# Performance work log

Measured on AMD Instinct MI355X. Metric: run time of the kernel, lower is better.

Reference implementation:

```python
import jax, jax.numpy as jnp
import numpy as np

N = 100000
E = 800000
D_IN = 128
D_H = 128
D_OUT = 40
L = 16
ALPHA = 0.1
THETA = 0.5
BN_EPS = 1e-5


def setup_inputs() -> dict:
    key = jax.random.key(0)
    ks = jax.random.split(key, 8)
    x = jax.random.normal(ks[0], (N, D_IN), dtype=jnp.float32)
    edge_row = jax.random.randint(ks[1], (E,), 0, N, dtype=jnp.int32)
    edge_col = jax.random.randint(ks[2], (E,), 0, N, dtype=jnp.int32)
    edge_weight = jax.random.uniform(ks[3], (E,), dtype=jnp.float32) / 8.0  # ~normalized adj values
    W_in = jax.random.normal(ks[4], (D_IN, D_H), dtype=jnp.float32) / np.sqrt(D_IN)
    b_in = jnp.zeros((D_H,), jnp.float32)
    conv_W = jax.random.normal(ks[5], (L, D_H, D_H), dtype=jnp.float32) / np.sqrt(D_H)
    bn_gamma = jnp.ones((L, D_H), jnp.float32)
    bn_beta = jnp.zeros((L, D_H), jnp.float32)
    W_out = jax.random.normal(ks[6], (D_H, D_OUT), dtype=jnp.float32) / np.sqrt(D_H)
    b_out = jnp.zeros((D_OUT,), jnp.float32)
    return {"x": x, "edge_weight": edge_weight, "W_in": W_in, "b_in": b_in,
            "conv_W": conv_W, "bn_gamma": bn_gamma, "bn_beta": bn_beta,
            "W_out": W_out, "b_out": b_out,
            "edge_row": edge_row, "edge_col": edge_col}


def reference(x, edge_weight, W_in, b_in, conv_W, bn_gamma, bn_beta, W_out, b_out, edge_row, edge_col):
    # input linear + relu (dropout p=0 -> identity)
    x0 = jax.nn.relu(x @ W_in + b_in)            # [N, D_H]
    # GCN2Conv beta coefficients: log(theta/layer + 1), layer = 1..L
    betas = jnp.log(THETA / jnp.arange(1, L + 1, dtype=jnp.float32) + 1.0)

    def spmm(h):
        # out[i] = sum_{e: row[e]=i} w[e] * h[col[e]]
        msgs = edge_weight[:, None] * h[edge_col]     # [E, D_H]
        return jax.ops.segment_sum(msgs, edge_row, num_segments=N)

    def layer(h, params):
        W, g, bb, beta = params
        a = spmm(h)                                   # propagate
        a = (1.0 - ALPHA) * a + ALPHA * x0            # initial-residual mix
        a = (1.0 - beta) * a + beta * (a @ W)         # shared-weights identity mapping
        mu = jnp.mean(a, axis=0)                      # BatchNorm1d (training stats)
        var = jnp.var(a, axis=0)
        a = (a - mu) * jax.lax.rsqrt(var + BN_EPS) * g + bb
        a = a + h                                     # residual
        return jax.nn.relu(a), None

    xL, _ = jax.lax.scan(layer, x0, (conv_W, bn_gamma, bn_beta, betas))
    return xL @ W_out + b_out                         # [N, D_OUT]
```

## Files before the change

kernel.cpp:

```cpp
#include <hip/hip_runtime.h>
#include <math.h>

#define NN 100000
#define EE 800000
#define DH 128
#define NL 16
#define GEMM_GRID 1563
#define SG_GRID 782
#define NSLOT 32

typedef __bf16 bf16x8 __attribute__((ext_vector_type(8)));
typedef float f32x4 __attribute__((ext_vector_type(4)));

__global__ void k_hist(const int* __restrict__ row, int* __restrict__ cnt) {
    int e = blockIdx.x * 256 + threadIdx.x;
    if (e < EE) atomicAdd(&cnt[__builtin_nontemporal_load(&row[e])], 1);
}

__global__ void k_scan1(const int* __restrict__ cnt, int* __restrict__ rp, int* __restrict__ part) {
    __shared__ int buf[512];
    int tid = threadIdx.x;
    int i = blockIdx.x * 512 + tid;
    int v = (i < NN) ? cnt[i] : 0;
    buf[tid] = v;
    __syncthreads();
    for (int off = 1; off < 512; off <<= 1) {
        int x = (tid >= off) ? buf[tid - off] : 0;
        __syncthreads();
        buf[tid] += x;
        __syncthreads();
    }
    if (i < NN) rp[i] = buf[tid] - v;
    if (tid == 511) part[blockIdx.x] = buf[511];
}

__global__ void k_scan2(int* __restrict__ part, int nparts) {
    __shared__ int buf[256];
    int tid = threadIdx.x;
    int v = (tid < nparts) ? part[tid] : 0;
    buf[tid] = v;
    __syncthreads();
    for (int off = 1; off < 256; off <<= 1) {
        int x = (tid >= off) ? buf[tid - off] : 0;
        __syncthreads();
        buf[tid] += x;
        __syncthreads();
    }
    if (tid < nparts) part[tid] = buf[tid] - v;
}

__global__ void k_scan3(int* __restrict__ rp, const int* __restrict__ part) {
    int i = blockIdx.x * 512 + threadIdx.x;
    if (i < NN) rp[i] += part[blockIdx.x];
    if (i == 0) rp[NN] = EE;
}

__global__ void k_dhist(const int* __restrict__ cnt, int* __restrict__ dbin) {
    __shared__ int lb[64];
    int tid = threadIdx.x;
    if (tid < 64) lb[tid] = 0;
    __syncthreads();
    int i = blockIdx.x * 256 + tid;
    if (i < NN) {
        int d = cnt[i];
        if (d > 63) d = 63;
        atomicAdd(&lb[63 - d], 1);
    }
    __syncthreads();
    if (tid < 64 && lb[tid]) atomicAdd(&dbin[tid], lb[tid]);
}

__global__ void k_pscan(const int* __restrict__ dbin, int* __restrict__ dpre) {
    if (threadIdx.x == 0) {
        int s = 0;
        for (int i = 0; i < 64; ++i) { dpre[i] = s; s += dbin[i]; }
    }
}

__global__ void k_pscatter(const int* __restrict__ cnt, const int* __restrict__ dpre,
                           int* __restrict__ dfil, int* __restrict__ perm) {
    __shared__ int lcnt[64], lbase[64];
    int tid = threadIdx.x;
    if (tid < 64) lcnt[tid] = 0;
    __syncthreads();
    int i = blockIdx.x * 256 + tid;
    int b = 0, loc = 0;
    bool ok = (i < NN);
    if (ok) {
        int d = cnt[i];
        if (d > 63) d = 63;
        b = 63 - d;
        loc = atomicAdd(&lcnt[b], 1);
    }
    __syncthreads();
    if (tid < 64 && lcnt[tid]) lbase[tid] = atomicAdd(&dfil[tid], lcnt[tid]);
    __syncthreads();
    if (ok) perm[dpre[b] + lbase[b] + loc] = i;
}

__global__ void k_iperm(const int* __restrict__ perm, const int* __restrict__ cnt,
                        int* __restrict__ iperm, int* __restrict__ cnt2) {
    int i = blockIdx.x * 256 + threadIdx.x;
    if (i < NN) {
        int p = perm[i];
        iperm[p] = i;
        cnt2[i] = cnt[p];
    }
}

__global__ void k_fill(const int* __restrict__ row, const int* __restrict__ col,
                       const float* __restrict__ w, const int* __restrict__ rp,
                       const int* __restrict__ iperm,
                       int* __restrict__ fil, int2* __restrict__ ep) {
    int e = blockIdx.x * 256 + threadIdx.x;
    if (e >= EE) return;
    int r = iperm[__builtin_nontemporal_load(&row[e])];
    int c = iperm[__builtin_nontemporal_load(&col[e])];
    float wv = 0.9f * __builtin_nontemporal_load(&w[e]);
    int pos = rp[r] + atomicAdd(&fil[r], 1);
    unsigned long long v = (unsigned long long)(unsigned)c |
                           ((unsigned long long)(unsigned)__float_as_int(wv) << 32);
    __builtin_nontemporal_store(v, (unsigned long long*)&ep[pos]);
}

__global__ void k_prep_w(const float* __restrict__ convW, const float* __restrict__ Win,
                         __bf16* __restrict__ Bhi, __bf16* __restrict__ Blo) {
    int l = blockIdx.x;
    const float* W;
    float beta, ob;
    if (l < NL) {
        beta = logf(0.5f / (float)(l + 1) + 1.0f);
        ob = 1.0f - beta;
        W = convW + (size_t)l * DH * DH;
    } else {
        beta = 1.0f;
        ob = 0.0f;
        W = Win;
    }
    __bf16* bh = Bhi + (size_t)l * DH * DH;
    __bf16* bl = Blo + (size_t)l * DH * DH;
    for (int i = threadIdx.x; i < DH * DH; i += 256) {
        int k = i >> 7, j = i & 127;
        float v = beta * W[i] + ((k == j) ? ob : 0.f);
        __bf16 hv = (__bf16)v;
        int t = j >> 4, n = j & 15, ks = k >> 5, quad = (k >> 3) & 3, e = k & 7;
        int off = ((t * 4 + ks) * 64 + quad * 16 + n) * 8 + e;
        bh[off] = hv;
        bl[off] = (__bf16)(v - (float)hv);
    }
}

__global__ void k_prep_out(const float* __restrict__ Wout, __bf16* __restrict__ Bhi, __bf16* __restrict__ Blo) {
    for (int i = threadIdx.x; i < DH * 48; i += 256) {
        int k = i / 48, j = i % 48;
        float v = (j < 40) ? Wout[k * 40 + j] : 0.f;
        __bf16 hv = (__bf16)v;
        int t = j >> 4, n = j & 15, ks = k >> 5, quad = (k >> 3) & 3, e = k & 7;
        int off = ((t * 4 + ks) * 64 + quad * 16 + n) * 8 + e;
        Bhi[off] = hv;
        Blo[off] = (__bf16)(v - (float)hv);
    }
}

__device__ inline void split8(const float* p, bf16x8& hi, bf16x8& lo) {
    f32x4 v0 = *(const f32x4*)p;
    f32x4 v1 = *(const f32x4*)(p + 4);
#pragma unroll
    for (int j = 0; j < 4; ++j) {
        __bf16 h0 = (__bf16)v0[j];
        hi[j] = h0;
        lo[j] = (__bf16)(v0[j] - (float)h0);
        __bf16 h1 = (__bf16)v1[j];
        hi[4 + j] = h1;
        lo[4 + j] = (__bf16)(v1[j] - (float)h1);
    }
}

#define MFMA(a, b, c) __builtin_amdgcn_mfma_f32_16x16x32_bf16(a, b, c, 0, 0, 0)

__device__ inline float dec_scale(unsigned int sc4, int ks) {
    return __uint_as_float(((sc4 >> (8 * ks)) & 0xffu) << 23);
}

#define DEC_DW(dw, wsv, a0, a1, a2, a3)                         \
    {                                                           \
        a0 = fmaf(wsv, (float)((dw)&0xffu), a0);                \
        a1 = fmaf(wsv, (float)(((dw) >> 8) & 0xffu), a1);       \
        a2 = fmaf(wsv, (float)(((dw) >> 16) & 0xffu), a2);      \
        a3 = fmaf(wsv, (float)((dw) >> 24), a3);                \
    }

#define EDGE_FMA(S4, W, RA, RB)                                       \
    {                                                                 \
        float _w = (W);                                               \
        float _w0 = _w * dec_scale(S4, 0);                            \
        float _w1 = _w * dec_scale(S4, 1);                            \
        float _w2 = _w * dec_scale(S4, 2);                            \
        float _w3 = _w * dec_scale(S4, 3);                            \
        sw0 += _w0; sw1 += _w1; sw2 += _w2; sw3 += _w3;               \
        DEC_DW((RA).x, _w0, acc[0][0], acc[0][1], acc[0][2], acc[0][3]); \
        DEC_DW((RA).y, _w0, acc[0][4], acc[0][5], acc[0][6], acc[0][7]); \
        DEC_DW((RA).z, _w1, acc[1][0], acc[1][1], acc[1][2], acc[1][3]); \
        DEC_DW((RA).w, _w1, acc[1][4], acc[1][5], acc[1][6], acc[1][7]); \
        DEC_DW((RB).x, _w2, acc[2][0], acc[2][1], acc[2][2], acc[2][3]); \
        DEC_DW((RB).y, _w2, acc[2][4], acc[2][5], acc[2][6], acc[2][7]); \
        DEC_DW((RB).z, _w3, acc[3][0], acc[3][1], acc[3][2], acc[3][3]); \
        DEC_DW((RB).w, _w3, acc[3][4], acc[3][5], acc[3][6], acc[3][7]); \
    }

__global__ __launch_bounds__(512, 4) void k_spmm_gemm(const unsigned char* __restrict__ hin8,
                                                      const unsigned char* __restrict__ hinsc,
                                                      const unsigned char* __restrict__ x08,
                                                      const unsigned char* __restrict__ x0sc,
                                                      const int* __restrict__ rp, const int2* __restrict__ ep,
                                                      unsigned char* __restrict__ a8, unsigned char* __restrict__ asc,
                                                      const __bf16* __restrict__ Bhi, const __bf16* __restrict__ Blo,
                                                      float* __restrict__ stats32) {
    __shared__ __bf16 Bs[2 * DH * DH];
    __shared__ float red[2][8][DH];
    int tid = threadIdx.x;
    {
        const f32x4* sh = (const f32x4*)Bhi;
        const f32x4* sl = (const f32x4*)Blo;
        f32x4* dh = (f32x4*)Bs;
        f32x4* dl = (f32x4*)(Bs + DH * DH);
#pragma unroll
        for (int i = 0; i < 4; ++i) {
            dh[tid + i * 512] = sh[tid + i * 512];
            dl[tid + i * 512] = sl[tid + i * 512];
        }
    }

    int wave = tid >> 6, lane = tid & 63;
    int n = lane & 15, quad = lane >> 4;
    int r0 = blockIdx.x * 128 + wave * 16;
    int node = r0 + n;
    int nc = (node < NN) ? node : (NN - 1);

    float acc[4][8];
#pragma unroll
    for (int ks = 0; ks < 4; ++ks)
#pragma unroll
        for (int c = 0; c < 8; ++c) acc[ks][c] = 0.f;
    float sw0 = 0.f, sw1 = 0.f, sw2 = 0.f, sw3 = 0.f;

    unsigned xs4 = *(const unsigned*)&x0sc[(size_t)nc * 4];
    const unsigned char* xb = x08 + (size_t)nc * 128 + quad * 16;
    uint4 xa = *(const uint4*)xb;
    uint4 xc = *(const uint4*)(xb + 64);

    int s = 0, e = 0;
    if (node < NN) { s = rp[node]; e = rp[node + 1]; }
    int cnt = e - s;
    int npairs = cnt >> 1;

    const unsigned char* hb = hin8 + quad * 16;

    int2 cP0, cP1, fP0, fP1;
    unsigned cS0, cS1;
    uint4 cA0, cB0, cA1, cB1;
    if (npairs > 0) {
        cP0 = ep[s]; cP1 = ep[s + 1];
        cS0 = *(const unsigned*)&hinsc[(size_t)cP0.x * 4];
        cS1 = *(const unsigned*)&hinsc[(size_t)cP1.x * 4];
        const unsigned char* b0 = hb + (size_t)cP0.x * 128;
        const unsigned char* b1 = hb + (size_t)cP1.x * 128;
        cA0 = *(const uint4*)b0; cB0 = *(const uint4*)(b0 + 64);
        cA1 = *(const uint4*)b1; cB1 = *(const uint4*)(b1 + 64);
        int jf = s + 2; if (jf > EE - 2) jf = EE - 2;
        fP0 = ep[jf]; fP1 = ep[jf + 1];
    }

    EDGE_FMA(xs4, 0.1f, xa, xc);

    int j = s;
    for (int it = 0; it < npairs; ++it) {
        int j2 = j + 4; if (j2 > EE - 2) j2 = EE - 2;
        int2 eN0 = ep[j2], eN1 = ep[j2 + 1];
        unsigned tS0 = *(const unsigned*)&hinsc[(size_t)fP0.x * 4];
        unsigned tS1 = *(const unsigned*)&hinsc[(size_t)fP1.x * 4];
        const unsigned char* b0 = hb + (size_t)fP0.x * 128;
        const unsigned char* b1 = hb + (size_t)fP1.x * 128;
        uint4 tA0 = *(const uint4*)b0, tB0 = *(const uint4*)(b0 + 64);
        uint4 tA1 = *(const uint4*)b1, tB1 = *(const uint4*)(b1 + 64);
        EDGE_FMA(cS0, __int_as_float(cP0.y), cA0, cB0);
        EDGE_FMA(cS1, __int_as_float(cP1.y), cA1, cB1);
        cP0 = fP0; cP1 = fP1; fP0 = eN0; fP1 = eN1;
        cS0 = tS0; cS1 = tS1;
        cA0 = tA0; cB0 = tB0; cA1 = tA1; cB1 = tB1;
        j += 2;
    }
    if (cnt & 1) {
        int2 pe = ep[e - 1];
        unsigned s4 = *(const unsigned*)&hinsc[(size_t)pe.x * 4];
        const unsigned char* bp = hb + (size_t)pe.x * 128;
        uint4 ra = *(const uint4*)bp, rb = *(const uint4*)(bp + 64);
        EDGE_FMA(s4, __int_as_float(pe.y), ra, rb);
    }

    bf16x8 av[4];
    {
        float sws[4] = {sw0, sw1, sw2, sw3};
#pragma unroll
        for (int ks = 0; ks < 4; ++ks)
#pragma unroll
            for (int c = 0; c < 8; ++c)
                av[ks][c] = (__bf16)(acc[ks][c] - 128.0f * sws[ks]);
    }

    __syncthreads();

    f32x4 gacc[8];
#pragma unroll
    for (int t = 0; t < 8; ++t) gacc[t] = (f32x4){0.f, 0.f, 0.f, 0.f};

#pragma unroll
    for (int ks = 0; ks < 4; ++ks) {
#pragma unroll
        for (int t = 0; t < 8; ++t) {
            int base = ((t * 4 + ks) * 64 + lane) * 8;
            bf16x8 bh = *(const bf16x8*)&Bs[base];
            bf16x8 bl = *(const bf16x8*)&Bs[DH * DH + base];
            gacc[t] = MFMA(av[ks], bh, gacc[t]);
            gacc[t] = MFMA(av[ks], bl, gacc[t]);
        }
    }

    float m[4][4];
#pragma unroll
    for (int r = 0; r < 4; ++r)
#pragma unroll
        for (int g = 0; g < 4; ++g)
            m[r][g] = fmaxf(fabsf(gacc[2 * g][r]), fabsf(gacc[2 * g + 1][r]));
#pragma unroll
    for (int d = 1; d <= 8; d <<= 1)
#pragma unroll
        for (int r = 0; r < 4; ++r)
#pragma unroll
            for (int g = 0; g < 4; ++g)
                m[r][g] = fmaxf(m[r][g], __shfl_xor(m[r][g], d));
    unsigned ebu[4];
    float sinv[4][4];
#pragma unroll
    for (int r = 0; r < 4; ++r) {
        unsigned u32 = 0;
#pragma unroll
        for (int g = 0; g < 4; ++g) {
            unsigned em = (__float_as_uint(m[r][g]) >> 23) & 0xffu;
            unsigned eb;
            float si;
            if (em < 7) { eb = 0; si = 0.f; }
            else { eb = em - 6; si = __uint_as_float((254 - eb) << 23); }
            u32 |= eb << (8 * g);
            sinv[r][g] = si;
        }
        ebu[r] = u32;
    }

#pragma unroll
    for (int t = 0; t < 8; ++t) {
        float sm = 0.f, qq = 0.f;
        int wb = (t >> 2) * 64 + ((((t & 1) << 1) | (n >> 3))) * 16 + ((t >> 1) & 1) * 8 + (n & 7);
#pragma unroll
        for (int r = 0; r < 4; ++r) {
            int row = r0 + quad * 4 + r;
            float v = gacc[t][r];
            if (row < NN) {
                unsigned qv = (unsigned)rintf(fminf(fmaf(v, sinv[r][t >> 1], 128.f), 255.f));
                a8[(size_t)row * 128 + wb] = (unsigned char)qv;
                sm += v;
                qq += v * v;
            }
        }
        sm += __shfl_xor(sm, 16); sm += __shfl_xor(sm, 32);
        qq += __shfl_xor(qq, 16); qq += __shfl_xor(qq, 32);
        if (quad == 0) {
            red[0][wave][t * 16 + n] = sm;
            red[1][wave][t * 16 + n] = qq;
        }
    }
    if (n == 0) {
#pragma unroll
        for (int r = 0; r < 4; ++r) {
            int row = r0 + quad * 4 + r;
            if (row < NN) *(unsigned*)&asc[(size_t)row * 4] = ebu[r];
        }
    }
    __syncthreads();
    if (tid < 256) {
        int which = tid >> 7, jj = tid & 127;
        float tot = 0.f;
#pragma unroll
        for (int w = 0; w < 8; ++w) tot += red[which][w][jj];
        atomicAdd(&stats32[(size_t)(blockIdx.x & (NSLOT - 1)) * 256 + tid], tot);
    }
}

__global__ __launch_bounds__(512, 4) void k_lin_in(const float* __restrict__ X, const int* __restrict__ perm,
                                                   const __bf16* __restrict__ Bhi, const __bf16* __restrict__ Blo,
                                                   const float* __restrict__ bin, __bf16* __restrict__ x0,
                                                   unsigned char* __restrict__ x08, unsigned char* __restrict__ xsc) {
    __shared__ __bf16 Bs[2 * DH * DH];
    int tid = threadIdx.x;
    {
        const f32x4* sh = (const f32x4*)Bhi;
        const f32x4* sl = (const f32x4*)Blo;
        f32x4* dh = (f32x4*)Bs;
        f32x4* dl = (f32x4*)(Bs + DH * DH);
#pragma unroll
        for (int i = 0; i < 4; ++i) {
            dh[tid + i * 512] = sh[tid + i * 512];
            dl[tid + i * 512] = sl[tid + i * 512];
        }
    }
    __syncthreads();

    int wave = tid >> 6, lane = tid & 63;
    int n = lane & 15, quad = lane >> 4;
    int r0 = blockIdx.x * 128 + wave * 16;
    int arow = r0 + n;
    if (arow > NN - 1) arow = NN - 1;
    const float* pa = X + (size_t)perm[arow] * DH + quad * 8;

    f32x4 acc[8];
#pragma unroll
    for (int t = 0; t < 8; ++t) acc[t] = (f32x4){0.f, 0.f, 0.f, 0.f};

#pragma unroll
    for (int ks = 0; ks < 4; ++ks) {
        bf16x8 ah, al;
        split8(pa + ks * 32, ah, al);
#pragma unroll
        for (int t = 0; t < 8; ++t) {
            int base = ((t * 4 + ks) * 64 + lane) * 8;
            bf16x8 bh = *(const bf16x8*)&Bs[base];
            bf16x8 bl = *(const bf16x8*)&Bs[DH * DH + base];
            acc[t] = MFMA(ah, bh, acc[t]);
            acc[t] = MFMA(al, bh, acc[t]);
            acc[t] = MFMA(ah, bl, acc[t]);
        }
    }

#pragma unroll
    for (int t = 0; t < 8; ++t) {
        float bj = bin[t * 16 + n];
#pragma unroll
        for (int r = 0; r < 4; ++r) {
            float v = fmaxf(acc[t][r] + bj, 0.f);
            acc[t][r] = v;
            int row = r0 + quad * 4 + r;
            if (row < NN) x0[(size_t)row * DH + t * 16 + n] = (__bf16)v;
        }
    }

    float m[4][4];
#pragma unroll
    for (int r = 0; r < 4; ++r)
#pragma unroll
        for (int g = 0; g < 4; ++g) {
            float v0 = (float)(__bf16)acc[2 * g][r];
            float v1 = (float)(__bf16)acc[2 * g + 1][r];
            m[r][g] = fmaxf(fabsf(v0), fabsf(v1));
        }
#pragma unroll
    for (int d = 1; d <= 8; d <<= 1)
#pragma unroll
        for (int r = 0; r < 4; ++r)
#pragma unroll
            for (int g = 0; g < 4; ++g)
                m[r][g] = fmaxf(m[r][g], __shfl_xor(m[r][g], d));
    unsigned ebu[4];
    float sinv[4][4];
#pragma unroll
    for (int r = 0; r < 4; ++r) {
        unsigned u32 = 0;
#pragma unroll
        for (int g = 0; g < 4; ++g) {
            unsigned em = (__float_as_uint(m[r][g]) >> 23) & 0xffu;
            unsigned eb;
            float si;
            if (em < 7) { eb = 0; si = 0.f; }
            else { eb = em - 6; si = __uint_as_float((254 - eb) << 23); }
            u32 |= eb << (8 * g);
            sinv[r][g] = si;
        }
        ebu[r] = u32;
    }
#pragma unroll
    for (int t = 0; t < 8; ++t) {
        int wb = (t >> 2) * 64 + ((((t & 1) << 1) | (n >> 3))) * 16 + ((t >> 1) & 1) * 8 + (n & 7);
#pragma unroll
        for (int r = 0; r < 4; ++r) {
            int row = r0 + quad * 4 + r;
            if (row < NN) {
                float v = (float)(__bf16)acc[t][r];
                unsigned qv = (unsigned)rintf(fminf(fmaf(v, sinv[r][t >> 1], 128.f), 255.f));
                x08[(size_t)row * 128 + wb] = (unsigned char)qv;
            }
        }
    }
    if (n == 0) {
#pragma unroll
        for (int r = 0; r < 4; ++r) {
            int row = r0 + quad * 4 + r;
            if (row < NN) *(unsigned*)&xsc[(size_t)row * 4] = ebu[r];
        }
    }
}

__global__ __launch_bounds__(256) void k_gemm_out(const __bf16* __restrict__ A, const int* __restrict__ perm,
                                                  const __bf16* __restrict__ Bhi, const __bf16* __restrict__ Blo,
                                                  const float* __restrict__ bout, float* __restrict__ out) {
    __shared__ __bf16 Bs[2 * 48 * DH];
    int tid = threadIdx.x;
    {
        const f32x4* sh = (const f32x4*)Bhi;
        const f32x4* sl = (const f32x4*)Blo;
        f32x4* dh = (f32x4*)Bs;
        f32x4* dl = (f32x4*)(Bs + 48 * DH);
#pragma unroll
        for (int i = 0; i < 3; ++i) {
            dh[tid + i * 256] = sh[tid + i * 256];
            dl[tid + i * 256] = sl[tid + i * 256];
        }
    }
    __syncthreads();

    int wave = tid >> 6, lane = tid & 63;
    int n = lane & 15, quad = lane >> 4;
    int r0 = blockIdx.x * 64 + wave * 16;
    int arow = r0 + n;
    if (arow > NN - 1) arow = NN - 1;
    const __bf16* pa = A + (size_t)arow * DH + quad * 8;

    f32x4 acc[3];
#pragma unroll
    for (int t = 0; t < 3; ++t) acc[t] = (f32x4){0.f, 0.f, 0.f, 0.f};

#pragma unroll
    for (int ks = 0; ks < 4; ++ks) {
        bf16x8 av = *(const bf16x8*)(pa + ks * 32);
#pragma unroll
        for (int t = 0; t < 3; ++t) {
            int base = ((t * 4 + ks) * 64 + lane) * 8;
            bf16x8 bh = *(const bf16x8*)&Bs[base];
            bf16x8 bl = *(const bf16x8*)&Bs[48 * DH + base];
            acc[t] = MFMA(av, bh, acc[t]);
            acc[t] = MFMA(av, bl, acc[t]);
        }
    }

    int prow[4];
#pragma unroll
    for (int r = 0; r < 4; ++r) {
        int row = r0 + quad * 4 + r;
        prow[r] = (row < NN) ? perm[row] : 0;
    }

#pragma unroll
    for (int t = 0; t < 3; ++t) {
        int j = t * 16 + n;
        float bj = (j < 40) ? bout[j] : 0.f;
#pragma unroll
        for (int r = 0; r < 4; ++r) {
            int row = r0 + quad * 4 + r;
            if (row < NN && j < 40) out[(size_t)prow[r] * 40 + j] = acc[t][r] + bj;
        }
    }
}

__global__ __launch_bounds__(256) void k_update(const unsigned char* __restrict__ a8,
                                                const unsigned char* __restrict__ asc,
                                                const __bf16* __restrict__ hin,
                                                __bf16* __restrict__ hout,
                                                unsigned char* __restrict__ h8, unsigned char* __restrict__ hsc,
                                                const float* __restrict__ stats32,
                                                const float* __restrict__ gamma, const float* __restrict__ bbeta) {
    __shared__ float scb[DH], shb[DH];
    int tid = threadIdx.x;
    if (tid < DH) {
        float s = 0.f, q = 0.f;
#pragma unroll
        for (int sl = 0; sl < NSLOT; ++sl) {
            s += stats32[(size_t)sl * 256 + tid];
            q += stats32[(size_t)sl * 256 + 128 + tid];
        }
        float mu = s * (1.0f / NN);
        float var = q * (1.0f / NN) - mu * mu;
        if (var < 0.f) var = 0.f;
        float sc = gamma[tid] * rsqrtf(var + 1e-5f);
        scb[tid] = sc;
        shb[tid] = bbeta[tid] - mu * sc;
    }
    __syncthreads();

    int idx = blockIdx.x * 256 + tid;
    int sub = idx & 15;
    int row = idx >> 4;
    int j0 = sub * 8;
    unsigned wpos = ((sub >> 3) & 1) * 64 + (sub & 3) * 16 + ((sub >> 2) & 1) * 8;
    uint2 ua = *(const uint2*)&a8[(size_t)row * 128 + wpos];
    float sA = dec_scale(*(const unsigned*)&asc[(size_t)row * 4], sub >> 2);
    bf16x8 hv = ((const bf16x8*)hin)[idx];
    bf16x8 o;
    float vv[8];
    float mx = 0.f;
#pragma unroll
    for (int c = 0; c < 8; ++c) {
        unsigned byte = ((c < 4 ? (ua.x >> (8 * c)) : (ua.y >> (8 * (c - 4)))) & 0xffu);
        float ad = ((float)byte - 128.f) * sA;
        int j = j0 + c;
        float v = fmaxf(fmaf(ad, scb[j], shb[j]) + (float)hv[c], 0.f);
        vv[c] = v;
        mx = fmaxf(mx, v);
        o[c] = (__bf16)v;
    }
    ((bf16x8*)hout)[idx] = o;

    mx = fmaxf(mx, __shfl_xor(mx, 1));
    mx = fmaxf(mx, __shfl_xor(mx, 2));
    unsigned int em = (__float_as_uint(mx) >> 23) & 0xffu;
    unsigned int eb;
    float sinv;
    if (em < 7) { eb = 0; sinv = 0.f; }
    else { eb = em - 6; sinv = __uint_as_float((254 - eb) << 23); }
    if ((tid & 3) == 0) hsc[(size_t)row * 4 + (sub >> 2)] = (unsigned char)eb;
    uint2 pk;
    pk.x = 0; pk.y = 0;
#pragma unroll
    for (int c = 0; c < 4; ++c) {
        unsigned int q0 = (unsigned int)rintf(fminf(fmaf(vv[c], sinv, 128.f), 255.f));
        unsigned int q1 = (unsigned int)rintf(fminf(fmaf(vv[4 + c], sinv, 128.f), 255.f));
        pk.x |= q0 << (8 * c);
        pk.y |= q1 << (8 * c);
    }
    *(uint2*)&h8[(size_t)row * 128 + wpos] = pk;
}

extern "C" void kernel_launch(void* const* d_in, const int* in_sizes, int n_in,
                              void* d_out, int out_size, void* d_ws, size_t ws_size,
                              hipStream_t stream) {
    const float* x = (const float*)d_in[0];
    const float* ew = (const float*)d_in[1];
    const float* Win = (const float*)d_in[2];
    const float* bin = (const float*)d_in[3];
    const float* convW = (const float*)d_in[4];
    const float* gamma = (const float*)d_in[5];
    const float* bbeta = (const float*)d_in[6];
    const float* Wout = (const float*)d_in[7];
    const float* bout = (const float*)d_in[8];
    const int* erow = (const int*)d_in[9];
    const int* ecol = (const int*)d_in[10];
    float* out = (float*)d_out;

    char* wsp = (char*)d_ws;
    size_t off = 0;
    auto alloc = [&](size_t bytes) -> void* {
        void* p = wsp + off;
        off += (bytes + 255) & ~(size_t)255;
        return p;
    };
    __bf16* x0 = (__bf16*)alloc((size_t)NN * DH * 2);
    __bf16* h = (__bf16*)alloc((size_t)NN * DH * 2);
    unsigned char* a8 = (unsigned char*)alloc((size_t)NN * DH);
    unsigned char* asc = (unsigned char*)alloc((size_t)NN * 4);
    unsigned char* x08 = (unsigned char*)alloc((size_t)NN * DH);
    unsigned char* h8 = (unsigned char*)alloc((size_t)NN * DH);
    unsigned char* x0sc = (unsigned char*)alloc((size_t)NN * 4);
    unsigned char* hsc = (unsigned char*)alloc((size_t)NN * 4);
    int* rp = (int*)alloc((NN + 1) * 4);
    int* perm = (int*)alloc((size_t)NN * 4);
    int* iperm = (int*)alloc((size_t)NN * 4);
    int* cnt2 = (int*)alloc((size_t)NN * 4);
    int* dpre = (int*)alloc(64 * 4);
    size_t zero_bytes = (size_t)NN * 4 + (size_t)NN * 4 + (size_t)NL * NSLOT * 256 * 4 + 128 * 4;
    int* cnt = (int*)alloc(zero_bytes);
    int* fil = cnt + NN;
    float* stats32 = (float*)(fil + NN);
    int* dbin = (int*)(stats32 + (size_t)NL * NSLOT * 256);
    int* dfil = dbin + 64;
    int2* ep = (int2*)alloc((size_t)EE * 8);
    int* part = (int*)alloc(256 * 4);
    __bf16* Bhi = (__bf16*)alloc((size_t)(NL + 1) * DH * DH * 2);
    __bf16* Blo = (__bf16*)alloc((size_t)(NL + 1) * DH * DH * 2);
    __bf16* Bohi = (__bf16*)alloc((size_t)DH * 48 * 2);
    __bf16* Bolo = (__bf16*)alloc((size_t)DH * 48 * 2);

    hipMemsetAsync(cnt, 0, zero_bytes, stream);

    k_hist<<<3125, 256, 0, stream>>>(erow, cnt);
    k_dhist<<<391, 256, 0, stream>>>(cnt, dbin);
    k_pscan<<<1, 64, 0, stream>>>(dbin, dpre);
    k_pscatter<<<391, 256, 0, stream>>>(cnt, dpre, dfil, perm);
    k_iperm<<<391, 256, 0, stream>>>(perm, cnt, iperm, cnt2);
    k_scan1<<<196, 512, 0, stream>>>(cnt2, rp, part);
    k_scan2<<<1, 256, 0, stream>>>(part, 196);
    k_scan3<<<196, 512, 0, stream>>>(rp, part);
    k_fill<<<3125, 256, 0, stream>>>(erow, ecol, ew, rp, iperm, fil, ep);

    k_prep_w<<<NL + 1, 256, 0, stream>>>(convW, Win, Bhi, Blo);
    k_prep_out<<<1, 256, 0, stream>>>(Wout, Bohi, Bolo);

    k_lin_in<<<SG_GRID, 512, 0, stream>>>(x, perm, Bhi + (size_t)NL * DH * DH, Blo + (size_t)NL * DH * DH,
                                          bin, x0, x08, x0sc);

    for (int l = 0; l < NL; ++l) {
        const unsigned char* hin8 = (l == 0) ? x08 : h8;
        const unsigned char* hinsc = (l == 0) ? x0sc : hsc;
        const __bf16* hin = (l == 0) ? x0 : h;
        float* st = stats32 + (size_t)l * NSLOT * 256;
        k_spmm_gemm<<<SG_GRID, 512, 0, stream>>>(hin8, hinsc, x08, x0sc, rp, ep, a8, asc,
                                                 Bhi + (size_t)l * DH * DH, Blo + (size_t)l * DH * DH, st);
        k_update<<<6250, 256, 0, stream>>>(a8, asc, hin, h, h8, hsc, st, gamma + l * DH, bbeta + l * DH);
    }
    k_gemm_out<<<GEMM_GRID, 256, 0, stream>>>(h, perm, Bohi, Bolo, bout, out);
}
```

Before: 1.193 ms.

## Store spmm-gemm output as bf16 and enlarge blocks to 1024 threads

The fused spmm+GEMM kernel now writes its per-layer output as plain bf16 instead of block-scaled int8 with per-row exponent scales. This removes the max-reduction and quantisation work there and the dequantisation in the update kernel, but doubles the bytes written and re-read for that intermediate. The block size doubles to 1024 threads covering 256 rows, with half the grid. The stats reduction buffer now reuses the weight shared memory after a barrier, so the extra reduction buffer is no longer needed.

```diff
diff --git a/kernel.cpp b/kernel.cpp
--- a/kernel.cpp
+++ b/kernel.cpp
@@ -7,6 +7,7 @@
 #define NL 16
 #define GEMM_GRID 1563
 #define SG_GRID 782
+#define SGQ_GRID 391
 #define NSLOT 32
 
 typedef __bf16 bf16x8 __attribute__((ext_vector_type(8)));
@@ -208,16 +209,15 @@
         DEC_DW((RB).w, _w3, acc[3][4], acc[3][5], acc[3][6], acc[3][7]); \
     }
 
-__global__ __launch_bounds__(512, 4) void k_spmm_gemm(const unsigned char* __restrict__ hin8,
-                                                      const unsigned char* __restrict__ hinsc,
-                                                      const unsigned char* __restrict__ x08,
-                                                      const unsigned char* __restrict__ x0sc,
-                                                      const int* __restrict__ rp, const int2* __restrict__ ep,
-                                                      unsigned char* __restrict__ a8, unsigned char* __restrict__ asc,
-                                                      const __bf16* __restrict__ Bhi, const __bf16* __restrict__ Blo,
-                                                      float* __restrict__ stats32) {
+__global__ __launch_bounds__(1024, 4) void k_spmm_gemm(const unsigned char* __restrict__ hin8,
+                                                       const unsigned char* __restrict__ hinsc,
+                                                       const unsigned char* __restrict__ x08,
+                                                       const unsigned char* __restrict__ x0sc,
+                                                       const int* __restrict__ rp, const int2* __restrict__ ep,
+                                                       __bf16* __restrict__ aout,
+                                                       const __bf16* __restrict__ Bhi, const __bf16* __restrict__ Blo,
+                                                       float* __restrict__ stats32) {
     __shared__ __bf16 Bs[2 * DH * DH];
-    __shared__ float red[2][8][DH];
     int tid = threadIdx.x;
     {
         const f32x4* sh = (const f32x4*)Bhi;
@@ -225,15 +225,15 @@
         f32x4* dh = (f32x4*)Bs;
         f32x4* dl = (f32x4*)(Bs + DH * DH);
 #pragma unroll
-        for (int i = 0; i < 4; ++i) {
-            dh[tid + i * 512] = sh[tid + i * 512];
-            dl[tid + i * 512] = sl[tid + i * 512];
+        for (int i = 0; i < 2; ++i) {
+            dh[tid + i * 1024] = sh[tid + i * 1024];
+            dl[tid + i * 1024] = sl[tid + i * 1024];
         }
     }
 
     int wave = tid >> 6, lane = tid & 63;
     int n = lane & 15, quad = lane >> 4;
-    int r0 = blockIdx.x * 128 + wave * 16;
+    int r0 = blockIdx.x * 256 + wave * 16;
     int node = r0 + n;
     int nc = (node < NN) ? node : (NN - 1);
 
@@ -326,12 +326,105 @@
         }
     }
 
+    __syncthreads();
+    float* red = (float*)Bs;
+
+#pragma unroll
+    for (int t = 0; t < 8; ++t) {
+        float sm = 0.f, qq = 0.f;
+#pragma unroll
+        for (int r = 0; r < 4; ++r) {
+            int row = r0 + quad * 4 + r;
+            float v = gacc[t][r];
+            if (row < NN) {
+                aout[(size_t)row * DH + t * 16 + n] = (__bf16)v;
+                sm += v;
+                qq += v * v;
+            }
+        }
+        sm += __shfl_xor(sm, 16); sm += __shfl_xor(sm, 32);
+        qq += __shfl_xor(qq, 16); qq += __shfl_xor(qq, 32);
+        if (quad == 0) {
+            red[(0 * 16 + wave) * DH + t * 16 + n] = sm;
+            red[(1 * 16 + wave) * DH + t * 16 + n] = qq;
+        }
+    }
+    __syncthreads();
+    if (tid < 256) {
+        int which = tid >> 7, jj = tid & 127;
+        float tot = 0.f;
+#pragma unroll
+        for (int w = 0; w < 16; ++w) tot += red[(which * 16 + w) * DH + jj];
+        atomicAdd(&stats32[(size_t)(blockIdx.x & (NSLOT - 1)) * 256 + tid], tot);
+    }
+}
+
+__global__ __launch_bounds__(512, 4) void k_lin_in(const float* __restrict__ X, const int* __restrict__ perm,
+                                                   const __bf16* __restrict__ Bhi, const __bf16* __restrict__ Blo,
+                                                   const float* __restrict__ bin, __bf16* __restrict__ x0,
+                                                   unsigned char* __restrict__ x08, unsigned char* __restrict__ xsc) {
+    __shared__ __bf16 Bs[2 * DH * DH];
+    int tid = threadIdx.x;
+    {
+        const f32x4* sh = (const f32x4*)Bhi;
+        const f32x4* sl = (const f32x4*)Blo;
+        f32x4* dh = (f32x4*)Bs;
+        f32x4* dl = (f32x4*)(Bs + DH * DH);
+#pragma unroll
+        for (int i = 0; i < 4; ++i) {
+            dh[tid + i * 512] = sh[tid + i * 512];
+            dl[tid + i * 512] = sl[tid + i * 512];
+        }
+    }
+    __syncthreads();
+
+    int wave = tid >> 6, lane = tid & 63;
+    int n = lane & 15, quad = lane >> 4;
+    int r0 = blockIdx.x * 128 + wave * 16;
+    int arow = r0 + n;
+    if (arow > NN - 1) arow = NN - 1;
+    const float* pa = X + (size_t)perm[arow] * DH + quad * 8;
+
+    f32x4 acc[8];
+#pragma unroll
+    for (int t = 0; t < 8; ++t) acc[t] = (f32x4){0.f, 0.f, 0.f, 0.f};
+
+#pragma unroll
+    for (int ks = 0; ks < 4; ++ks) {
+        bf16x8 ah, al;
+        split8(pa + ks * 32, ah, al);
+#pragma unroll
+        for (int t = 0; t < 8; ++t) {
+            int base = ((t * 4 + ks) * 64 + lane) * 8;
+            bf16x8 bh = *(const bf16x8*)&Bs[base];
+            bf16x8 bl = *(const bf16x8*)&Bs[DH * DH + base];
+            acc[t] = MFMA(ah, bh, acc[t]);
+            acc[t] = MFMA(al, bh, acc[t]);
+            acc[t] = MFMA(ah, bl, acc[t]);
+        }
+    }
+
+#pragma unroll
+    for (int t = 0; t < 8; ++t) {
+        float bj = bin[t * 16 + n];
+#pragma unroll
+        for (int r = 0; r < 4; ++r) {
+            float v = fmaxf(acc[t][r] + bj, 0.f);
+            acc[t][r] = v;
+            int row = r0 + quad * 4 + r;
+            if (row < NN) x0[(size_t)row * DH + t * 16 + n] = (__bf16)v;
+        }
+    }
+
     float m[4][4];
 #pragma unroll
     for (int r = 0; r < 4; ++r)
 #pragma unroll
-        for (int g = 0; g < 4; ++g)
-            m[r][g] = fmaxf(fabsf(gacc[2 * g][r]), fabsf(gacc[2 * g + 1][r]));
+        for (int g = 0; g < 4; ++g) {
+            float v0 = (float)(__bf16)acc[2 * g][r];
+            float v1 = (float)(__bf16)acc[2 * g + 1][r];
+            m[r][g] = fmaxf(fabsf(v0), fabsf(v1));
+        }
 #pragma unroll
     for (int d = 1; d <= 8; d <<= 1)
 #pragma unroll
@@ -356,136 +449,6 @@
         }
         ebu[r] = u32;
     }
-
-#pragma unroll
-    for (int t = 0; t < 8; ++t) {
-        float sm = 0.f, qq = 0.f;
-        int wb = (t >> 2) * 64 + ((((t & 1) << 1) | (n >> 3))) * 16 + ((t >> 1) & 1) * 8 + (n & 7);
-#pragma unroll
-        for (int r = 0; r < 4; ++r) {
-            int row = r0 + quad * 4 + r;
-            float v = gacc[t][r];
-            if (row < NN) {
-                unsigned qv = (unsigned)rintf(fminf(fmaf(v, sinv[r][t >> 1], 128.f), 255.f));
-                a8[(size_t)row * 128 + wb] = (unsigned char)qv;
-                sm += v;
-                qq += v * v;
-            }
-        }
-        sm += __shfl_xor(sm, 16); sm += __shfl_xor(sm, 32);
-        qq += __shfl_xor(qq, 16); qq += __shfl_xor(qq, 32);
-        if (quad == 0) {
-            red[0][wave][t * 16 + n] = sm;
-            red[1][wave][t * 16 + n] = qq;
-        }
-    }
-    if (n == 0) {
-#pragma unroll
-        for (int r = 0; r < 4; ++r) {
-            int row = r0 + quad * 4 + r;
-            if (row < NN) *(unsigned*)&asc[(size_t)row * 4] = ebu[r];
-        }
-    }
-    __syncthreads();
-    if (tid < 256) {
-        int which = tid >> 7, jj = tid & 127;
-        float tot = 0.f;
-#pragma unroll
-        for (int w = 0; w < 8; ++w) tot += red[which][w][jj];
-        atomicAdd(&stats32[(size_t)(blockIdx.x & (NSLOT - 1)) * 256 + tid], tot);
-    }
-}
-
-__global__ __launch_bounds__(512, 4) void k_lin_in(const float* __restrict__ X, const int* __restrict__ perm,
-                                                   const __bf16* __restrict__ Bhi, const __bf16* __restrict__ Blo,
-                                                   const float* __restrict__ bin, __bf16* __restrict__ x0,
-                                                   unsigned char* __restrict__ x08, unsigned char* __restrict__ xsc) {
-    __shared__ __bf16 Bs[2 * DH * DH];
-    int tid = threadIdx.x;
-    {
-        const f32x4* sh = (const f32x4*)Bhi;
-        const f32x4* sl = (const f32x4*)Blo;
-        f32x4* dh = (f32x4*)Bs;
-        f32x4* dl = (f32x4*)(Bs + DH * DH);
-#pragma unroll
-        for (int i = 0; i < 4; ++i) {
-            dh[tid + i * 512] = sh[tid + i * 512];
-            dl[tid + i * 512] = sl[tid + i * 512];
-        }
-    }
-    __syncthreads();
-
-    int wave = tid >> 6, lane = tid & 63;
-    int n = lane & 15, quad = lane >> 4;
-    int r0 = blockIdx.x * 128 + wave * 16;
-    int arow = r0 + n;
-    if (arow > NN - 1) arow = NN - 1;
-    const float* pa = X + (size_t)perm[arow] * DH + quad * 8;
-
-    f32x4 acc[8];
-#pragma unroll
-    for (int t = 0; t < 8; ++t) acc[t] = (f32x4){0.f, 0.f, 0.f, 0.f};
-
-#pragma unroll
-    for (int ks = 0; ks < 4; ++ks) {
-        bf16x8 ah, al;
-        split8(pa + ks * 32, ah, al);
-#pragma unroll
-        for (int t = 0; t < 8; ++t) {
-            int base = ((t * 4 + ks) * 64 + lane) * 8;
-            bf16x8 bh = *(const bf16x8*)&Bs[base];
-            bf16x8 bl = *(const bf16x8*)&Bs[DH * DH + base];
-            acc[t] = MFMA(ah, bh, acc[t]);
-            acc[t] = MFMA(al, bh, acc[t]);
-            acc[t] = MFMA(ah, bl, acc[t]);
-        }
-    }
-
-#pragma unroll
-    for (int t = 0; t < 8; ++t) {
-        float bj = bin[t * 16 + n];
-#pragma unroll
-        for (int r = 0; r < 4; ++r) {
-            float v = fmaxf(acc[t][r] + bj, 0.f);
-            acc[t][r] = v;
-            int row = r0 + quad * 4 + r;
-            if (row < NN) x0[(size_t)row * DH + t * 16 + n] = (__bf16)v;
-        }
-    }
-
-    float m[4][4];
-#pragma unroll
-    for (int r = 0; r < 4; ++r)
-#pragma unroll
-        for (int g = 0; g < 4; ++g) {
-            float v0 = (float)(__bf16)acc[2 * g][r];
-            float v1 = (float)(__bf16)acc[2 * g + 1][r];
-            m[r][g] = fmaxf(fabsf(v0), fabsf(v1));
-        }
-#pragma unroll
-    for (int d = 1; d <= 8; d <<= 1)
-#pragma unroll
-        for (int r = 0; r < 4; ++r)
-#pragma unroll
-            for (int g = 0; g < 4; ++g)
-                m[r][g] = fmaxf(m[r][g], __shfl_xor(m[r][g], d));
-    unsigned ebu[4];
-    float sinv[4][4];
-#pragma unroll
-    for (int r = 0; r < 4; ++r) {
-        unsigned u32 = 0;
-#pragma unroll
-        for (int g = 0; g < 4; ++g) {
-            unsigned em = (__float_as_uint(m[r][g]) >> 23) & 0xffu;
-            unsigned eb;
-            float si;
-            if (em < 7) { eb = 0; si = 0.f; }
-            else { eb = em - 6; si = __uint_as_float((254 - eb) << 23); }
-            u32 |= eb << (8 * g);
-            sinv[r][g] = si;
-        }
-        ebu[r] = u32;
-    }
 #pragma unroll
     for (int t = 0; t < 8; ++t) {
         int wb = (t >> 2) * 64 + ((((t & 1) << 1) | (n >> 3))) * 16 + ((t >> 1) & 1) * 8 + (n & 7);
@@ -569,9 +532,7 @@
     }
 }
 
-__global__ __launch_bounds__(256) void k_update(const unsigned char* __restrict__ a8,
-                                                const unsigned char* __restrict__ asc,
-                                                const __bf16* __restrict__ hin,
+__global__ __launch_bounds__(256) void k_update(const __bf16* __restrict__ a, const __bf16* __restrict__ hin,
                                                 __bf16* __restrict__ hout,
                                                 unsigned char* __restrict__ h8, unsigned char* __restrict__ hsc,
                                                 const float* __restrict__ stats32,
@@ -596,21 +557,16 @@
 
     int idx = blockIdx.x * 256 + tid;
     int sub = idx & 15;
-    int row = idx >> 4;
     int j0 = sub * 8;
-    unsigned wpos = ((sub >> 3) & 1) * 64 + (sub & 3) * 16 + ((sub >> 2) & 1) * 8;
-    uint2 ua = *(const uint2*)&a8[(size_t)row * 128 + wpos];
-    float sA = dec_scale(*(const unsigned*)&asc[(size_t)row * 4], sub >> 2);
+    bf16x8 av = ((const bf16x8*)a)[idx];
     bf16x8 hv = ((const bf16x8*)hin)[idx];
     bf16x8 o;
     float vv[8];
     float mx = 0.f;
 #pragma unroll
     for (int c = 0; c < 8; ++c) {
-        unsigned byte = ((c < 4 ? (ua.x >> (8 * c)) : (ua.y >> (8 * (c - 4)))) & 0xffu);
-        float ad = ((float)byte - 128.f) * sA;
         int j = j0 + c;
-        float v = fmaxf(fmaf(ad, scb[j], shb[j]) + (float)hv[c], 0.f);
+        float v = fmaxf(fmaf((float)av[c], scb[j], shb[j]) + (float)hv[c], 0.f);
         vv[c] = v;
         mx = fmaxf(mx, v);
         o[c] = (__bf16)v;
@@ -624,7 +580,7 @@
     float sinv;
     if (em < 7) { eb = 0; sinv = 0.f; }
     else { eb = em - 6; sinv = __uint_as_float((254 - eb) << 23); }
-    if ((tid & 3) == 0) hsc[(size_t)row * 4 + (sub >> 2)] = (unsigned char)eb;
+    if ((tid & 3) == 0) hsc[(size_t)(idx >> 4) * 4 + (sub >> 2)] = (unsigned char)eb;
     uint2 pk;
     pk.x = 0; pk.y = 0;
 #pragma unroll
@@ -634,7 +590,8 @@
         pk.x |= q0 << (8 * c);
         pk.y |= q1 << (8 * c);
     }
-    *(uint2*)&h8[(size_t)row * 128 + wpos] = pk;
+    unsigned wpos = ((sub >> 3) & 1) * 64 + (sub & 3) * 16 + ((sub >> 2) & 1) * 8;
+    *(uint2*)&h8[(size_t)(idx >> 4) * 128 + wpos] = pk;
 }
 
 extern "C" void kernel_launch(void* const* d_in, const int* in_sizes, int n_in,
@@ -662,8 +619,7 @@
     };
     __bf16* x0 = (__bf16*)alloc((size_t)NN * DH * 2);
     __bf16* h = (__bf16*)alloc((size_t)NN * DH * 2);
-    unsigned char* a8 = (unsigned char*)alloc((size_t)NN * DH);
-    unsigned char* asc = (unsigned char*)alloc((size_t)NN * 4);
+    __bf16* a = (__bf16*)alloc((size_t)NN * DH * 2);
     unsigned char* x08 = (unsigned char*)alloc((size_t)NN * DH);
     unsigned char* h8 = (unsigned char*)alloc((size_t)NN * DH);
     unsigned char* x0sc = (unsigned char*)alloc((size_t)NN * 4);
@@ -709,9 +665,9 @@
         const unsigned char* hinsc = (l == 0) ? x0sc : hsc;
         const __bf16* hin = (l == 0) ? x0 : h;
         float* st = stats32 + (size_t)l * NSLOT * 256;
-        k_spmm_gemm<<<SG_GRID, 512, 0, stream>>>(hin8, hinsc, x08, x0sc, rp, ep, a8, asc,
-                                                 Bhi + (size_t)l * DH * DH, Blo + (size_t)l * DH * DH, st);
-        k_update<<<6250, 256, 0, stream>>>(a8, asc, hin, h, h8, hsc, st, gamma + l * DH, bbeta + l * DH);
+        k_spmm_gemm<<<SGQ_GRID, 1024, 0, stream>>>(hin8, hinsc, x08, x0sc, rp, ep, a,
+                                                   Bhi + (size_t)l * DH * DH, Blo + (size_t)l * DH * DH, st);
+        k_update<<<6250, 256, 0, stream>>>(a, hin, h, h8, hsc, st, gamma + l * DH, bbeta + l * DH);
     }
     k_gemm_out<<<GEMM_GRID, 256, 0, stream>>>(h, perm, Bohi, Bolo, bout, out);
 }
```

Measured after the change: 1.162 ms. 2.6% less time.
